# Performance work log

Hardware: AMD Instinct MI355X
Metric: run time of the kernel (lower is better)

## Reference

```python
import jax, jax.numpy as jnp
import numpy as np

K, R, D = 200000, 64, 1024
N_IDS = 16384
BITS = 4
GROUP = 32


def group_quantize(w, bits, group_size):
    """Group-wise symmetric fake-quant along the last dim (STE in bwd)."""
    last = w.shape[-1]
    g = min(group_size, last)
    n_groups = last // g
    wg = w.reshape(w.shape[:-1] + (n_groups, g))
    amax = jnp.clip(jnp.max(jnp.abs(wg), axis=-1, keepdims=True), 1e-8, None)
    q_max = (1 << (bits - 1)) - 1  # matches torch `1 << bits - 1` precedence
    scale = amax / q_max
    q = jnp.clip(jnp.round(wg / scale), -q_max, q_max) * scale
    # straight-through estimator: forward = q, backward = identity w.r.t. wg
    wq = wg + jax.lax.stop_gradient(q - wg)
    return wq.reshape(w.shape)


def setup_inputs() -> dict:
    key = jax.random.key(0)
    k1, k2, k3 = jax.random.split(key, 3)
    U = jax.random.normal(k1, (K, R), dtype=jnp.float32)
    B = jax.random.normal(k2, (R, D), dtype=jnp.float32)
    local_ids = jax.random.randint(k3, (N_IDS,), 0, K, dtype=jnp.int64 if jax.config.read('jax_enable_x64') else jnp.int32)
    return {"U": U, "B": B, "local_ids": local_ids}


def reference(U, B, local_ids):
    # row(): quantize ALL of U, gather selected rows, matmul with quantized B
    Uq = group_quantize(U, BITS, min(GROUP, R))   # [K, r]
    Bq = group_quantize(B, BITS, min(GROUP, D))   # [r, d]
    return Uq[local_ids] @ Bq                      # [N, d]
```

## Files before the change

kernel.cpp:

```cpp
#include <hip/hip_runtime.h>


#define R_DIM 64
#define D_DIM 1024
#define N_IDS 16384

#define BM 64
#define BN 64
#define LDS_STRIDE 72
#define OT_STRIDE 68

typedef __attribute__((ext_vector_type(8))) __bf16 bf16x8;
typedef __attribute__((ext_vector_type(4))) float f32x4;

__device__ inline unsigned short f32_to_bf16_rne(float f) {
  union { float f; unsigned int u; } c; c.f = f;
  unsigned int u = c.u;
  u += 0x7fffu + ((u >> 16) & 1u);
  return (unsigned short)(u >> 16);
}

__device__ inline float bf16_bits_to_f32(unsigned short h) {
  union { unsigned int u; float f; } c; c.u = ((unsigned int)h) << 16;
  return c.f;
}

__device__ inline void quant_elem(float w, double scale,
                                  unsigned short* hi, unsigned short* lo) {
  double t = (double)w / scale;
  double q = fmin(fmax(rint(t), -7.0), 7.0) * scale;
  float qf = (float)q;
  unsigned short h = f32_to_bf16_rne(qf);
  *hi = h;
  *lo = f32_to_bf16_rne(qf - bf16_bits_to_f32(h));
}

__global__ __launch_bounds__(256) void quantB_kernel(
    const float* __restrict__ B,
    unsigned short* __restrict__ BqT_hi, unsigned short* __restrict__ BqT_lo) {
  int e4 = blockIdx.x * 256 + threadIdx.x;
  int e  = e4 * 4;
  int r  = e >> 10;
  int c  = e & 1023;
  float4 w = *(const float4*)(B + e);
  float a = fmaxf(fmaxf(fabsf(w.x), fabsf(w.y)), fmaxf(fabsf(w.z), fabsf(w.w)));
  a = fmaxf(a, __shfl_xor(a, 1));
  a = fmaxf(a, __shfl_xor(a, 2));
  a = fmaxf(a, __shfl_xor(a, 4));
  double sc = fmax((double)a, 1e-8) / 7.0;
  float wv[4] = {w.x, w.y, w.z, w.w};
  #pragma unroll
  for (int j = 0; j < 4; ++j) {
    unsigned short hi, lo;
    quant_elem(wv[j], sc, &hi, &lo);
    BqT_hi[(c + j) * R_DIM + r] = hi;
    BqT_lo[(c + j) * R_DIM + r] = lo;
  }
}

__global__ __launch_bounds__(256, 8) void gemm_kernel(
    const float* __restrict__ U, const int* __restrict__ ids,
    const unsigned short* __restrict__ BqT_hi, const unsigned short* __restrict__ BqT_lo,
    float* __restrict__ out) {
  __shared__ char smem[2 * BN * LDS_STRIDE * 2];
  unsigned short* bt_hi = (unsigned short*)smem;
  unsigned short* bt_lo = bt_hi + BN * LDS_STRIDE;
  float* ot = (float*)smem;

  const int tid  = threadIdx.x;
  const int lane = tid & 63;
  const int wave = tid >> 6;
  const int bx   = blockIdx.x;
  const int nb   = bx & 15;
  const int mb   = bx >> 4;
  const int n0   = nb * BN;
  const int m0   = mb * BM + wave * 16;
  const int koff  = (lane >> 4) * 8;
  const int nlane = lane & 15;

  const float* urow = U + (size_t)ids[m0 + nlane] * R_DIM;
  float4 wr[2][2];
  #pragma unroll
  for (int s = 0; s < 2; ++s) {
    wr[s][0] = *(const float4*)(urow + s * 32 + koff);
    wr[s][1] = *(const float4*)(urow + s * 32 + koff + 4);
  }

  {
    const uint4* src_hi = (const uint4*)(BqT_hi + (size_t)n0 * R_DIM);
    const uint4* src_lo = (const uint4*)(BqT_lo + (size_t)n0 * R_DIM);
    #pragma unroll
    for (int it = 0; it < 2; ++it) {
      int c = tid + it * 256;
      int row = c >> 3, off = c & 7;
      *(uint4*)&bt_hi[row * LDS_STRIDE + off * 8] = src_hi[c];
      *(uint4*)&bt_lo[row * LDS_STRIDE + off * 8] = src_lo[c];
    }
  }

  bf16x8 ah[2], al[2];
  #pragma unroll
  for (int s = 0; s < 2; ++s) {
    float4 w0 = wr[s][0], w1 = wr[s][1];
    float wv[8] = {w0.x, w0.y, w0.z, w0.w, w1.x, w1.y, w1.z, w1.w};
    float a = 0.0f;
    #pragma unroll
    for (int j = 0; j < 8; ++j) a = fmaxf(a, fabsf(wv[j]));
    a = fmaxf(a, __shfl_xor(a, 16));
    a = fmaxf(a, __shfl_xor(a, 32));
    double sc = fmax((double)a, 1e-8) / 7.0;
    union { unsigned short s8[8]; bf16x8 b; } uh, ul;
    #pragma unroll
    for (int j = 0; j < 8; ++j) {
      unsigned short hi, lo;
      quant_elem(wv[j], sc, &hi, &lo);
      uh.s8[j] = hi;
      ul.s8[j] = lo;
    }
    ah[s] = uh.b;
    al[s] = ul.b;
  }

  __syncthreads();

  f32x4 acc[4];
  #pragma unroll
  for (int nf = 0; nf < 4; ++nf) acc[nf] = (f32x4){0.f, 0.f, 0.f, 0.f};

  #pragma unroll
  for (int nf = 0; nf < 4; ++nf) {
    #pragma unroll
    for (int s = 0; s < 2; ++s) {
      const int boff = (nf * 16 + nlane) * LDS_STRIDE + s * 32 + koff;
      union { uint4 u; bf16x8 b; } bh, bl;
      bh.u = *(const uint4*)&bt_hi[boff];
      bl.u = *(const uint4*)&bt_lo[boff];
      acc[nf] = __builtin_amdgcn_mfma_f32_16x16x32_bf16(ah[s], bh.b, acc[nf], 0, 0, 0);
      acc[nf] = __builtin_amdgcn_mfma_f32_16x16x32_bf16(ah[s], bl.b, acc[nf], 0, 0, 0);
      acc[nf] = __builtin_amdgcn_mfma_f32_16x16x32_bf16(al[s], bh.b, acc[nf], 0, 0, 0);
    }
  }

  __syncthreads();

  float* wp = ot + wave * 16 * OT_STRIDE;
  {
    const int r0 = (lane >> 4) << 2;
    #pragma unroll
    for (int nf = 0; nf < 4; ++nf) {
      #pragma unroll
      for (int i = 0; i < 4; ++i) {
        wp[(r0 + i) * OT_STRIDE + nlane + nf * 16] = acc[nf][i];
      }
    }
  }
  #pragma unroll
  for (int j = 0; j < 4; ++j) {
    const int row = j * 4 + (lane >> 4);
    f32x4 v = *(const f32x4*)&wp[row * OT_STRIDE + nlane * 4];
    __builtin_nontemporal_store(v,
        (f32x4*)&out[(size_t)(m0 + row) * D_DIM + n0 + nlane * 4]);
  }
}

extern "C" void kernel_launch(void* const* d_in, const int* in_sizes, int n_in,
                              void* d_out, int out_size, void* d_ws, size_t ws_size,
                              hipStream_t stream) {
  const float* U   = (const float*)d_in[0];
  const float* B   = (const float*)d_in[1];
  const int*   ids = (const int*)d_in[2];
  float* out = (float*)d_out;

  unsigned short* BqT_hi = (unsigned short*)d_ws;
  unsigned short* BqT_lo = BqT_hi + R_DIM * D_DIM;

  quantB_kernel<<<(R_DIM * D_DIM) / (256 * 4), 256, 0, stream>>>(B, BqT_hi, BqT_lo);
  gemm_kernel<<<(N_IDS / BM) * (D_DIM / BN), 256, 0, stream>>>(U, ids, BqT_hi, BqT_lo, out);
}
```

Measured before the change: 32.69 us.

## Widen gemm tiles to reuse quantized U rows; use float fast-path quantization

Each gemm block now covers 256 output columns as two 128-column slices, so every gathered and quantized U row is reused across four times more columns. This cuts the redundant U gathers and quantization work and shrinks the grid from 4096 to 1024 blocks. Quantization now uses a float reciprocal multiply and rint, and falls back to the exact double divide only near rounding ties, to avoid double-precision work. The cost is fewer blocks for latency hiding, lower occupancy from larger LDS and register tiles, and serialized load/compute/store per slice.

```diff
diff --git a/kernel.cpp b/kernel.cpp
--- a/kernel.cpp
+++ b/kernel.cpp
@@ -6,9 +6,10 @@
 #define N_IDS 16384
 
 #define BM 64
-#define BN 64
+#define BN 128
+#define NSLICE 2
 #define LDS_STRIDE 72
-#define OT_STRIDE 68
+#define OT_STRIDE 132
 
 typedef __attribute__((ext_vector_type(8))) __bf16 bf16x8;
 typedef __attribute__((ext_vector_type(4))) float f32x4;
@@ -25,11 +26,18 @@
   return c.f;
 }
 
-__device__ inline void quant_elem(float w, double scale,
-                                  unsigned short* hi, unsigned short* lo) {
-  double t = (double)w / scale;
-  double q = fmin(fmax(rint(t), -7.0), 7.0) * scale;
-  float qf = (float)q;
+__device__ inline void quant_elem_g(float w, float rcp32, double scale_d,
+                                    unsigned short* hi, unsigned short* lo) {
+  float t32 = w * rcp32;
+  float n32 = rintf(t32);
+  double n;
+  if (__builtin_expect(fabsf(fabsf(t32 - n32) - 0.5f) < 1e-4f, 0)) {
+    n = rint((double)w / scale_d);
+  } else {
+    n = (double)n32;
+  }
+  n = fmin(fmax(n, -7.0), 7.0);
+  float qf = (float)(n * scale_d);
   unsigned short h = f32_to_bf16_rne(qf);
   *hi = h;
   *lo = f32_to_bf16_rne(qf - bf16_bits_to_f32(h));
@@ -48,17 +56,18 @@
   a = fmaxf(a, __shfl_xor(a, 2));
   a = fmaxf(a, __shfl_xor(a, 4));
   double sc = fmax((double)a, 1e-8) / 7.0;
+  float rcp = 1.0f / (float)sc;
   float wv[4] = {w.x, w.y, w.z, w.w};
   #pragma unroll
   for (int j = 0; j < 4; ++j) {
     unsigned short hi, lo;
-    quant_elem(wv[j], sc, &hi, &lo);
+    quant_elem_g(wv[j], rcp, sc, &hi, &lo);
     BqT_hi[(c + j) * R_DIM + r] = hi;
     BqT_lo[(c + j) * R_DIM + r] = lo;
   }
 }
 
-__global__ __launch_bounds__(256, 8) void gemm_kernel(
+__global__ __launch_bounds__(256, 4) void gemm_kernel(
     const float* __restrict__ U, const int* __restrict__ ids,
     const unsigned short* __restrict__ BqT_hi, const unsigned short* __restrict__ BqT_lo,
     float* __restrict__ out) {
@@ -71,9 +80,8 @@
   const int lane = tid & 63;
   const int wave = tid >> 6;
   const int bx   = blockIdx.x;
-  const int nb   = bx & 15;
-  const int mb   = bx >> 4;
-  const int n0   = nb * BN;
+  const int grp  = bx & 3;
+  const int mb   = bx >> 2;
   const int m0   = mb * BM + wave * 16;
   const int koff  = (lane >> 4) * 8;
   const int nlane = lane & 15;
@@ -86,18 +94,6 @@
     wr[s][1] = *(const float4*)(urow + s * 32 + koff + 4);
   }
 
-  {
-    const uint4* src_hi = (const uint4*)(BqT_hi + (size_t)n0 * R_DIM);
-    const uint4* src_lo = (const uint4*)(BqT_lo + (size_t)n0 * R_DIM);
-    #pragma unroll
-    for (int it = 0; it < 2; ++it) {
-      int c = tid + it * 256;
-      int row = c >> 3, off = c & 7;
-      *(uint4*)&bt_hi[row * LDS_STRIDE + off * 8] = src_hi[c];
-      *(uint4*)&bt_lo[row * LDS_STRIDE + off * 8] = src_lo[c];
-    }
-  }
-
   bf16x8 ah[2], al[2];
   #pragma unroll
   for (int s = 0; s < 2; ++s) {
@@ -108,12 +104,13 @@
     for (int j = 0; j < 8; ++j) a = fmaxf(a, fabsf(wv[j]));
     a = fmaxf(a, __shfl_xor(a, 16));
     a = fmaxf(a, __shfl_xor(a, 32));
-    double sc = fmax((double)a, 1e-8) / 7.0;
+    const double sc = fmax((double)a, 1e-8) / 7.0;
+    const float rcp = 1.0f / (float)sc;
     union { unsigned short s8[8]; bf16x8 b; } uh, ul;
     #pragma unroll
     for (int j = 0; j < 8; ++j) {
       unsigned short hi, lo;
-      quant_elem(wv[j], sc, &hi, &lo);
+      quant_elem_g(wv[j], rcp, sc, &hi, &lo);
       uh.s8[j] = hi;
       ul.s8[j] = lo;
     }
@@ -121,45 +118,63 @@
     al[s] = ul.b;
   }
 
-  __syncthreads();
+  #pragma unroll
+  for (int sl = 0; sl < NSLICE; ++sl) {
+    const int n0 = (grp * NSLICE + sl) * BN;
 
-  f32x4 acc[4];
-  #pragma unroll
-  for (int nf = 0; nf < 4; ++nf) acc[nf] = (f32x4){0.f, 0.f, 0.f, 0.f};
+    if (sl > 0) __syncthreads();
 
-  #pragma unroll
-  for (int nf = 0; nf < 4; ++nf) {
-    #pragma unroll
-    for (int s = 0; s < 2; ++s) {
-      const int boff = (nf * 16 + nlane) * LDS_STRIDE + s * 32 + koff;
-      union { uint4 u; bf16x8 b; } bh, bl;
-      bh.u = *(const uint4*)&bt_hi[boff];
-      bl.u = *(const uint4*)&bt_lo[boff];
-      acc[nf] = __builtin_amdgcn_mfma_f32_16x16x32_bf16(ah[s], bh.b, acc[nf], 0, 0, 0);
-      acc[nf] = __builtin_amdgcn_mfma_f32_16x16x32_bf16(ah[s], bl.b, acc[nf], 0, 0, 0);
-      acc[nf] = __builtin_amdgcn_mfma_f32_16x16x32_bf16(al[s], bh.b, acc[nf], 0, 0, 0);
-    }
-  }
-
-  __syncthreads();
-
-  float* wp = ot + wave * 16 * OT_STRIDE;
-  {
-    const int r0 = (lane >> 4) << 2;
-    #pragma unroll
-    for (int nf = 0; nf < 4; ++nf) {
+    {
+      const uint4* src_hi = (const uint4*)(BqT_hi + (size_t)n0 * R_DIM);
+      const uint4* src_lo = (const uint4*)(BqT_lo + (size_t)n0 * R_DIM);
       #pragma unroll
-      for (int i = 0; i < 4; ++i) {
-        wp[(r0 + i) * OT_STRIDE + nlane + nf * 16] = acc[nf][i];
+      for (int it = 0; it < 4; ++it) {
+        int c = tid + it * 256;
+        int row = c >> 3, off = c & 7;
+        *(uint4*)&bt_hi[row * LDS_STRIDE + off * 8] = src_hi[c];
+        *(uint4*)&bt_lo[row * LDS_STRIDE + off * 8] = src_lo[c];
       }
     }
-  }
-  #pragma unroll
-  for (int j = 0; j < 4; ++j) {
-    const int row = j * 4 + (lane >> 4);
-    f32x4 v = *(const f32x4*)&wp[row * OT_STRIDE + nlane * 4];
-    __builtin_nontemporal_store(v,
-        (f32x4*)&out[(size_t)(m0 + row) * D_DIM + n0 + nlane * 4]);
+    __syncthreads();
+
+    f32x4 acc[8];
+    #pragma unroll
+    for (int nf = 0; nf < 8; ++nf) acc[nf] = (f32x4){0.f, 0.f, 0.f, 0.f};
+
+    #pragma unroll
+    for (int nf = 0; nf < 8; ++nf) {
+      #pragma unroll
+      for (int s = 0; s < 2; ++s) {
+        const int boff = (nf * 16 + nlane) * LDS_STRIDE + s * 32 + koff;
+        union { uint4 u; bf16x8 b; } bh, bl;
+        bh.u = *(const uint4*)&bt_hi[boff];
+        bl.u = *(const uint4*)&bt_lo[boff];
+        acc[nf] = __builtin_amdgcn_mfma_f32_16x16x32_bf16(ah[s], bh.b, acc[nf], 0, 0, 0);
+        acc[nf] = __builtin_amdgcn_mfma_f32_16x16x32_bf16(ah[s], bl.b, acc[nf], 0, 0, 0);
+        acc[nf] = __builtin_amdgcn_mfma_f32_16x16x32_bf16(al[s], bh.b, acc[nf], 0, 0, 0);
+      }
+    }
+
+    __syncthreads();
+
+    float* wp = ot + wave * 16 * OT_STRIDE;
+    {
+      const int r0 = (lane >> 4) << 2;
+      #pragma unroll
+      for (int nf = 0; nf < 8; ++nf) {
+        #pragma unroll
+        for (int i = 0; i < 4; ++i) {
+          wp[(r0 + i) * OT_STRIDE + nlane + nf * 16] = acc[nf][i];
+        }
+      }
+    }
+    #pragma unroll
+    for (int j = 0; j < 8; ++j) {
+      const int row = j * 2 + (lane >> 5);
+      f32x4 v = *(const f32x4*)&wp[row * OT_STRIDE + (lane & 31) * 4];
+      __builtin_nontemporal_store(v,
+          (f32x4*)&out[(size_t)(m0 + row) * D_DIM + n0 + (lane & 31) * 4]);
+    }
   }
 }
 
@@ -175,5 +190,6 @@
   unsigned short* BqT_lo = BqT_hi + R_DIM * D_DIM;
 
   quantB_kernel<<<(R_DIM * D_DIM) / (256 * 4), 256, 0, stream>>>(B, BqT_hi, BqT_lo);
-  gemm_kernel<<<(N_IDS / BM) * (D_DIM / BN), 256, 0, stream>>>(U, ids, BqT_hi, BqT_lo, out);
+  gemm_kernel<<<(N_IDS / BM) * (D_DIM / (BN * NSLICE)), 256, 0, stream>>>(
+      U, ids, BqT_hi, BqT_lo, out);
 }
```

Measured after the change: 30.55 us. -6.6%, faster.
